# Performance work log

Measured on AMD Instinct MI355X. Metric: run time of the kernel, lower is better.

## Reference

```python
import jax, jax.numpy as jnp
import numpy as np

N = 50000   # num_nodes
E = 400000  # num_edges
IN, HID, OUT, H = 128, 64, 128, 4
GAT_HID = HID * H  # 256
EPS = 1e-5
NEG_SLOPE = 0.2


def setup_inputs() -> dict:
    key = jax.random.key(0)
    ks = jax.random.split(key, 24)

    def w(k, shape, fan_in):
        return (jax.random.normal(k, shape) * (1.0 / np.sqrt(fan_in))).astype(jnp.float32)

    x = jax.random.normal(ks[0], (N, IN), dtype=jnp.float32)
    edge_index = jax.random.randint(ks[1], (2, E), 0, N, dtype=jnp.int32)

    return {
        "x": x,
        "edge_index": edge_index,
        # GCN branch: layer1 IN->HID, layer2 HID->OUT
        "W_gcn1": w(ks[2], (IN, HID), IN), "b_gcn1": jnp.zeros((HID,), jnp.float32),
        "W_gcn2": w(ks[3], (HID, OUT), HID), "b_gcn2": jnp.zeros((OUT,), jnp.float32),
        # GAT branch: layer1 IN -> H heads x HID (concat), layer2 GAT_HID -> H heads x OUT (mean)
        "W_gat1": w(ks[4], (IN, H * HID), IN),
        "a_src1": w(ks[5], (H, HID), HID), "a_dst1": w(ks[6], (H, HID), HID),
        "b_gat1": jnp.zeros((H * HID,), jnp.float32),
        "W_gat2": w(ks[7], (GAT_HID, H * OUT), GAT_HID),
        "a_src2": w(ks[8], (H, OUT), OUT), "a_dst2": w(ks[9], (H, OUT), OUT),
        "b_gat2": jnp.zeros((OUT,), jnp.float32),
        # LayerNorms
        "g_gcn": jnp.ones((OUT,), jnp.float32), "bt_gcn": jnp.zeros((OUT,), jnp.float32),
        "g_gat": jnp.ones((OUT,), jnp.float32), "bt_gat": jnp.zeros((OUT,), jnp.float32),
        # projected_concat fusion
        "W_fuse": w(ks[10], (2 * OUT, OUT), 2 * OUT), "b_fuse": jnp.zeros((OUT,), jnp.float32),
    }


def _with_self_loops(src, dst, n):
    loop = jnp.arange(n, dtype=src.dtype)
    return jnp.concatenate([src, loop]), jnp.concatenate([dst, loop])


def _gcn_layer(x, W, b, src, dst, n):
    # PyG GCNConv: x' = D^{-1/2}(A+I)D^{-1/2} X W + b
    xw = x @ W
    s, d = _with_self_loops(src, dst, n)
    deg = jax.ops.segment_sum(jnp.ones_like(s, dtype=xw.dtype), d, num_segments=n)
    dis = jnp.where(deg > 0, jax.lax.rsqrt(jnp.maximum(deg, 1.0)), 0.0)
    norm = dis[s] * dis[d]                      # [E2]
    msg = norm[:, None] * xw[s]                 # [E2, C]
    return jax.ops.segment_sum(msg, d, num_segments=n) + b


def _segment_softmax(e, seg, n):
    m = jax.ops.segment_max(e, seg, num_segments=n)
    ee = jnp.exp(e - m[seg])
    den = jax.ops.segment_sum(ee, seg, num_segments=n)
    return ee / den[seg]


def _gat_layer(x, W, a_src, a_dst, b, src, dst, n, heads, out_ch, concat):
    xh = (x @ W).reshape(n, heads, out_ch)      # [N, H, C]
    alpha_s = jnp.einsum('nhc,hc->nh', xh, a_src)
    alpha_d = jnp.einsum('nhc,hc->nh', xh, a_dst)
    s, d = _with_self_loops(src, dst, n)
    e = jax.nn.leaky_relu(alpha_s[s] + alpha_d[d], NEG_SLOPE)   # [E2, H]
    alpha = _segment_softmax(e, d, n)                           # [E2, H]
    out = jax.ops.segment_sum(alpha[:, :, None] * xh[s], d, num_segments=n)  # [N,H,C]
    if concat:
        return out.reshape(n, heads * out_ch) + b
    return out.mean(axis=1) + b


def _layer_norm(x, g, b):
    mu = x.mean(axis=-1, keepdims=True)
    var = ((x - mu) ** 2).mean(axis=-1, keepdims=True)
    return (x - mu) * jax.lax.rsqrt(var + EPS) * g + b


def reference(x, edge_index,
              W_gcn1, b_gcn1, W_gcn2, b_gcn2,
              W_gat1, a_src1, a_dst1, b_gat1,
              W_gat2, a_src2, a_dst2, b_gat2,
              g_gcn, bt_gcn, g_gat, bt_gat,
              W_fuse, b_fuse):
    src, dst = edge_index[0], edge_index[1]
    n = x.shape[0]
    # GCN branch (relu between layers, dropout p=0.0 -> identity)
    h = jax.nn.relu(_gcn_layer(x, W_gcn1, b_gcn1, src, dst, n))
    x_gcn = _gcn_layer(h, W_gcn2, b_gcn2, src, dst, n)
    # GAT branch (elu between layers)
    g1 = _gat_layer(x, W_gat1, a_src1, a_dst1, b_gat1, src, dst, n, H, HID, True)
    g1 = jax.nn.elu(g1)
    x_gat = _gat_layer(g1, W_gat2, a_src2, a_dst2, b_gat2, src, dst, n, H, OUT, False)
    # Norm + projected_concat fusion
    x_gcn = _layer_norm(x_gcn, g_gcn, bt_gcn)
    x_gat = _layer_norm(x_gat, g_gat, bt_gat)
    x_cat = jnp.concatenate([x_gcn, x_gat], axis=-1)
    return x_cat @ W_fuse + b_fuse
```

## Files before the change

kernel.cpp:

```cpp
#include <hip/hip_runtime.h>
#include <cmath>

static constexpr float EPS = 1e-5f;
static constexpr float NEG = 0.2f;

typedef __attribute__((ext_vector_type(8))) short short8v;
typedef __attribute__((ext_vector_type(4))) short short4v;
typedef __attribute__((ext_vector_type(4))) float f32x4;

__device__ inline unsigned short f2bf(float f) {
    union { float f; unsigned u; } v; v.f = f;
    unsigned r = v.u + 0x7FFF + ((v.u >> 16) & 1);
    return (unsigned short)(r >> 16);
}
__device__ inline float bf2f(unsigned short u) {
    union { unsigned u; float f; } v; v.u = (unsigned)u << 16; return v.f;
}

__global__ void setup_kernel(const int* __restrict__ ei, int* __restrict__ cnt, int E, int n,
                             const float* __restrict__ x, unsigned short* __restrict__ xb,
                             const float* W1, const float* W2, const float* W3,
                             const float* W4, const float* W5,
                             unsigned short* T1, unsigned short* T2, unsigned short* T3,
                             unsigned short* TF, unsigned short* T5,
                             const float* as1, const float* ad1,
                             const float* as2, const float* ad2,
                             float* wa1, float* wa2) {
    int gid = blockIdx.x * 256 + threadIdx.x;
    if (gid < E) {
        atomicAdd(&cnt[ei[E + gid]], 1);
        return;
    }
    gid -= E;
    int n32 = n * 32;
    if (gid < n32) {
        float4 v = *reinterpret_cast<const float4*>(&x[(size_t)gid * 4]);
        unsigned long long pk = (unsigned long long)f2bf(v.x)
                              | ((unsigned long long)f2bf(v.y) << 16)
                              | ((unsigned long long)f2bf(v.z) << 32)
                              | ((unsigned long long)f2bf(v.w) << 48);
        *reinterpret_cast<unsigned long long*>(&xb[(size_t)gid * 4]) = pk;
        return;
    }
    gid -= n32;
    if (gid < 212992) {
        int idx = gid;
        if (idx < 8192) {
            int c = idx / 128, k = idx % 128;
            T1[idx] = f2bf(W1[(size_t)k * 64 + c]);
        } else if (idx < 16384) {
            int j = idx - 8192, c = j / 64, k = j % 64;
            T2[j] = f2bf(W2[(size_t)k * 128 + c]);
        } else if (idx < 49152) {
            int j = idx - 16384, c = j / 128, k = j % 128;
            T3[j] = f2bf(W3[(size_t)k * 256 + c]);
        } else if (idx < 180224) {
            int j = idx - 49152;
            int c = j / 1024, kk = j % 1024, h = kk >> 8, k = kk & 255;
            TF[j] = f2bf(0.25f * W4[(size_t)k * 512 + h * 128 + c]);
        } else {
            int j = idx - 180224, c = j / 256, k = j % 256;
            T5[j] = f2bf(W5[(size_t)k * 128 + c]);
        }
        return;
    }
    gid -= 212992;
    if (gid < 1024) {
        int k = gid >> 3, t = gid & 7, h = t >> 1;
        const float* a = (t & 1) ? ad1 : as1;
        float s = 0.f;
        for (int c = 0; c < 64; c++) s += W3[(size_t)k * 256 + h * 64 + c] * a[h * 64 + c];
        wa1[gid] = s;
    } else if (gid < 3072) {
        int j = gid - 1024;
        int k = j >> 3, t = j & 7, h = t >> 1;
        const float* a = (t & 1) ? ad2 : as2;
        float s = 0.f;
        for (int c = 0; c < 128; c++) s += W4[(size_t)k * 512 + h * 128 + c] * a[h * 128 + c];
        wa2[j] = s;
    }
}

__global__ __launch_bounds__(256) void partial_kernel(const int* __restrict__ cnt,
                                                      int* __restrict__ partials, int n) {
    int tid = threadIdx.x, lane = tid & 63, wid = tid >> 6;
    int base = blockIdx.x * 1024 + tid * 4;
    int s = 0;
    if (base + 3 < n) {
        int4 v = *reinterpret_cast<const int4*>(&cnt[base]);
        s = v.x + v.y + v.z + v.w;
    } else {
        for (int j = 0; j < 4; j++) if (base + j < n) s += cnt[base + j];
    }
    #pragma unroll
    for (int o = 32; o; o >>= 1) s += __shfl_xor(s, o, 64);
    __shared__ int ws[4];
    if (lane == 0) ws[wid] = s;
    __syncthreads();
    if (tid == 0) partials[blockIdx.x] = ws[0] + ws[1] + ws[2] + ws[3];
}

__global__ void scanp_kernel(int* __restrict__ partials, int nb) {
    int lane = threadIdx.x;
    int v = (lane < nb) ? partials[lane] : 0;
    int s = v;
    #pragma unroll
    for (int o = 1; o < 64; o <<= 1) {
        int t = __shfl_up(s, o, 64);
        if (lane >= o) s += t;
    }
    if (lane < nb) partials[lane] = s - v;
}

__global__ __launch_bounds__(256) void scan2_kernel(const int* __restrict__ cnt,
                                                    const int* __restrict__ partials,
                                                    int* __restrict__ rowptr,
                                                    int* __restrict__ cursor,
                                                    float* __restrict__ dis, int n, int E) {
    int tid = threadIdx.x, lane = tid & 63, wid = tid >> 6;
    int base = blockIdx.x * 1024 + tid * 4;
    int v[4]; int s = 0;
    #pragma unroll
    for (int j = 0; j < 4; j++) { v[j] = (base + j < n) ? cnt[base + j] : 0; s += v[j]; }
    int ts = s;
    #pragma unroll
    for (int o = 1; o < 64; o <<= 1) {
        int t = __shfl_up(ts, o, 64);
        if (lane >= o) ts += t;
    }
    __shared__ int wsum[4];
    if (lane == 63) wsum[wid] = ts;
    __syncthreads();
    int woff = 0;
    for (int w = 0; w < wid; w++) woff += wsum[w];
    int excl = ts - s + woff + partials[blockIdx.x];
    #pragma unroll
    for (int j = 0; j < 4; j++) {
        int idx = base + j;
        if (idx < n) {
            rowptr[idx] = excl;
            cursor[idx] = excl;
            dis[idx] = rsqrtf((float)(v[j] + 1));
            excl += v[j];
        }
    }
    if (blockIdx.x == 0 && tid == 0) rowptr[n] = E;
}

__global__ void fill_kernel(const int* __restrict__ ei, int* __restrict__ cursor,
                            int* __restrict__ col, int E) {
    int e = blockIdx.x * 256 + threadIdx.x;
    if (e < E) {
        int d = ei[E + e];
        int pos = atomicAdd(&cursor[d], 1);
        col[pos] = ei[e];
    }
}

template<int BM, int K, int C, bool OBF>
__global__ __launch_bounds__(256) void mfma_gemm(const unsigned short* __restrict__ A,
                                                 const unsigned short* __restrict__ WT,
                                                 const float* __restrict__ bias,
                                                 void* __restrict__ outp, int M) {
    constexpr int BN = 64, BK = 64;
    constexpr int MF = BM / 64;
    __shared__ unsigned short As[BM * BK];
    __shared__ unsigned short Ws[BN * BK];
    int tid = threadIdx.x;
    int wid = tid >> 6, lane = tid & 63;
    int m0 = blockIdx.x * BM;
    int n0 = blockIdx.y * BN;

    f32x4 acc[MF][4] = {};

    for (int k0 = 0; k0 < K; k0 += BK) {
        for (int i = tid; i < BM * (BK / 8); i += 256) {
            int row = i >> 3;
            int kk = (i & 7) * 8;
            int gr = m0 + row;
            short8v v = short8v{0, 0, 0, 0, 0, 0, 0, 0};
            if (gr < M) v = *reinterpret_cast<const short8v*>(&A[(size_t)gr * K + k0 + kk]);
            int byte = (kk * 2) ^ ((row & 7) << 4);
            *reinterpret_cast<short8v*>((char*)As + row * (BK * 2) + byte) = v;
        }
        for (int i = tid; i < BN * (BK / 8); i += 256) {
            int nrow = i >> 3;
            int kk = (i & 7) * 8;
            short8v v = *reinterpret_cast<const short8v*>(&WT[(size_t)(n0 + nrow) * K + k0 + kk]);
            int byte = (kk * 2) ^ ((nrow & 7) << 4);
            *reinterpret_cast<short8v*>((char*)Ws + nrow * (BK * 2) + byte) = v;
        }
        __syncthreads();
        #pragma unroll
        for (int kc = 0; kc < BK; kc += 32) {
            short8v afr[MF], bfr[4];
            int kk = kc + (lane >> 4) * 8;
            #pragma unroll
            for (int mf = 0; mf < MF; mf++) {
                int row = wid * (16 * MF) + mf * 16 + (lane & 15);
                int byte = (kk * 2) ^ ((row & 7) << 4);
                afr[mf] = *reinterpret_cast<const short8v*>((char*)As + row * (BK * 2) + byte);
            }
            #pragma unroll
            for (int nf = 0; nf < 4; nf++) {
                int nrow = nf * 16 + (lane & 15);
                int byte = (kk * 2) ^ ((nrow & 7) << 4);
                bfr[nf] = *reinterpret_cast<const short8v*>((char*)Ws + nrow * (BK * 2) + byte);
            }
            #pragma unroll
            for (int mf = 0; mf < MF; mf++)
                #pragma unroll
                for (int nf = 0; nf < 4; nf++)
                    acc[mf][nf] = __builtin_amdgcn_mfma_f32_16x16x32_bf16(
                        afr[mf], bfr[nf], acc[mf][nf], 0, 0, 0);
        }
        __syncthreads();
    }
    #pragma unroll
    for (int mf = 0; mf < MF; mf++) {
        #pragma unroll
        for (int nf = 0; nf < 4; nf++) {
            #pragma unroll
            for (int r = 0; r < 4; r++) {
                int row = m0 + wid * (16 * MF) + mf * 16 + (lane >> 4) * 4 + r;
                int colg = n0 + nf * 16 + (lane & 15);
                if (row < M) {
                    float v = acc[mf][nf][r];
                    if (bias) v += bias[colg];
                    if constexpr (OBF)
                        ((unsigned short*)outp)[(size_t)row * C + colg] = f2bf(v);
                    else
                        ((float*)outp)[(size_t)row * C + colg] = v;
                }
            }
        }
    }
}

__global__ __launch_bounds__(256) void gemm_head_kernel(const unsigned short* __restrict__ A,
                                                        const unsigned short* __restrict__ WT3,
                                                        const float* __restrict__ bias,
                                                        unsigned short* __restrict__ g1b, int M) {
    constexpr int BM = 64, BK = 64, K = 128;
    int head = blockIdx.y;
    __shared__ unsigned short As[BM * BK];
    __shared__ unsigned short Ws[64 * BK];
    int tid = threadIdx.x;
    int wid = tid >> 6, lane = tid & 63;
    int m0 = blockIdx.x * BM;

    f32x4 acc[4] = {};

    for (int k0 = 0; k0 < K; k0 += BK) {
        for (int i = tid; i < BM * (BK / 8); i += 256) {
            int row = i >> 3;
            int kk = (i & 7) * 8;
            int gr = m0 + row;
            short8v v = short8v{0, 0, 0, 0, 0, 0, 0, 0};
            if (gr < M) v = *reinterpret_cast<const short8v*>(&A[(size_t)gr * 512 + head * 128 + k0 + kk]);
            int byte = (kk * 2) ^ ((row & 7) << 4);
            *reinterpret_cast<short8v*>((char*)As + row * (BK * 2) + byte) = v;
        }
        for (int i = tid; i < 64 * (BK / 8); i += 256) {
            int nrow = i >> 3;
            int kk = (i & 7) * 8;
            short8v v = *reinterpret_cast<const short8v*>(&WT3[(size_t)(head * 64 + nrow) * 128 + k0 + kk]);
            int byte = (kk * 2) ^ ((nrow & 7) << 4);
            *reinterpret_cast<short8v*>((char*)Ws + nrow * (BK * 2) + byte) = v;
        }
        __syncthreads();
        #pragma unroll
        for (int kc = 0; kc < BK; kc += 32) {
            short8v afr, bfr[4];
            int kk = kc + (lane >> 4) * 8;
            {
                int row = wid * 16 + (lane & 15);
                int byte = (kk * 2) ^ ((row & 7) << 4);
                afr = *reinterpret_cast<const short8v*>((char*)As + row * (BK * 2) + byte);
            }
            #pragma unroll
            for (int nf = 0; nf < 4; nf++) {
                int nrow = nf * 16 + (lane & 15);
                int byte = (kk * 2) ^ ((nrow & 7) << 4);
                bfr[nf] = *reinterpret_cast<const short8v*>((char*)Ws + nrow * (BK * 2) + byte);
            }
            #pragma unroll
            for (int nf = 0; nf < 4; nf++)
                acc[nf] = __builtin_amdgcn_mfma_f32_16x16x32_bf16(afr, bfr[nf], acc[nf], 0, 0, 0);
        }
        __syncthreads();
    }
    #pragma unroll
    for (int nf = 0; nf < 4; nf++) {
        #pragma unroll
        for (int r = 0; r < 4; r++) {
            int row = m0 + wid * 16 + (lane >> 4) * 4 + r;
            int cl = head * 64 + nf * 16 + (lane & 15);
            if (row < M) {
                float v = acc[nf][r] + bias[cl];
                v = v > 0.f ? v : __expf(v) - 1.f;
                g1b[(size_t)row * 256 + cl] = f2bf(v);
            }
        }
    }
}

template<int K>
__global__ __launch_bounds__(256) void gemm_ln_kernel(const unsigned short* __restrict__ A,
                                                      const unsigned short* __restrict__ WT,
                                                      const float* __restrict__ bias,
                                                      const float* __restrict__ gw,
                                                      const float* __restrict__ gb,
                                                      unsigned short* __restrict__ catb,
                                                      int coloff, int M) {
    constexpr int BM = 64, BN = 128, BK = 64;
    __shared__ unsigned short As[BM * BK];
    __shared__ unsigned short Ws[BN * BK];
    int tid = threadIdx.x;
    int wid = tid >> 6, lane = tid & 63;
    int m0 = blockIdx.x * BM;

    f32x4 acc[8] = {};

    for (int k0 = 0; k0 < K; k0 += BK) {
        for (int i = tid; i < BM * (BK / 8); i += 256) {
            int row = i >> 3;
            int kk = (i & 7) * 8;
            int gr = m0 + row;
            short8v v = short8v{0, 0, 0, 0, 0, 0, 0, 0};
            if (gr < M) v = *reinterpret_cast<const short8v*>(&A[(size_t)gr * K + k0 + kk]);
            int byte = (kk * 2) ^ ((row & 7) << 4);
            *reinterpret_cast<short8v*>((char*)As + row * (BK * 2) + byte) = v;
        }
        for (int i = tid; i < BN * (BK / 8); i += 256) {
            int nrow = i >> 3;
            int kk = (i & 7) * 8;
            short8v v = *reinterpret_cast<const short8v*>(&WT[(size_t)nrow * K + k0 + kk]);
            int byte = (kk * 2) ^ ((nrow & 7) << 4);
            *reinterpret_cast<short8v*>((char*)Ws + nrow * (BK * 2) + byte) = v;
        }
        __syncthreads();
        #pragma unroll
        for (int kc = 0; kc < BK; kc += 32) {
            short8v afr, bfr[8];
            int kk = kc + (lane >> 4) * 8;
            {
                int row = wid * 16 + (lane & 15);
                int byte = (kk * 2) ^ ((row & 7) << 4);
                afr = *reinterpret_cast<const short8v*>((char*)As + row * (BK * 2) + byte);
            }
            #pragma unroll
            for (int nf = 0; nf < 8; nf++) {
                int nrow = nf * 16 + (lane & 15);
                int byte = (kk * 2) ^ ((nrow & 7) << 4);
                bfr[nf] = *reinterpret_cast<const short8v*>((char*)Ws + nrow * (BK * 2) + byte);
            }
            #pragma unroll
            for (int nf = 0; nf < 8; nf++)
                acc[nf] = __builtin_amdgcn_mfma_f32_16x16x32_bf16(afr, bfr[nf], acc[nf], 0, 0, 0);
        }
        __syncthreads();
    }
    int cb = lane & 15;
    float gwv[8], gbv[8], bv[8];
    #pragma unroll
    for (int nf = 0; nf < 8; nf++) {
        int c = nf * 16 + cb;
        gwv[nf] = gw[c]; gbv[nf] = gb[c]; bv[nf] = bias[c];
    }
    #pragma unroll
    for (int r = 0; r < 4; r++) {
        int row = m0 + wid * 16 + (lane >> 4) * 4 + r;
        float v[8]; float sm = 0.f, sq = 0.f;
        #pragma unroll
        for (int nf = 0; nf < 8; nf++) {
            v[nf] = acc[nf][r] + bv[nf];
            sm += v[nf]; sq += v[nf] * v[nf];
        }
        #pragma unroll
        for (int o = 1; o < 16; o <<= 1) { sm += __shfl_xor(sm, o, 64); sq += __shfl_xor(sq, o, 64); }
        float mu = sm * (1.f / 128.f);
        float var = sq * (1.f / 128.f) - mu * mu;
        float rs = rsqrtf(var + EPS);
        if (row < M) {
            #pragma unroll
            for (int nf = 0; nf < 8; nf++)
                catb[(size_t)row * 256 + coloff + nf * 16 + cb] =
                    f2bf((v[nf] - mu) * rs * gwv[nf] + gbv[nf]);
        }
    }
}

template<int K>
__global__ __launch_bounds__(256) void alpha_x_kernel(const unsigned short* __restrict__ F,
                                                      const float* __restrict__ wa,
                                                      float* __restrict__ as_, float* __restrict__ ad_, int n) {
    constexpr int PL = K / 64;
    int wid = threadIdx.x >> 6, lane = threadIdx.x & 63;
    int node = blockIdx.x * 4 + wid;
    if (node >= n) return;
    float p[8] = {0, 0, 0, 0, 0, 0, 0, 0};
    const unsigned short* fr = F + (size_t)node * K + lane * PL;
    #pragma unroll
    for (int j = 0; j < PL; j++) {
        float v = bf2f(fr[j]);
        const float4* w4 = reinterpret_cast<const float4*>(wa + (size_t)(lane * PL + j) * 8);
        float4 wA = w4[0], wB = w4[1];
        p[0] += v * wA.x; p[1] += v * wA.y; p[2] += v * wA.z; p[3] += v * wA.w;
        p[4] += v * wB.x; p[5] += v * wB.y; p[6] += v * wB.z; p[7] += v * wB.w;
    }
    #pragma unroll
    for (int o = 1; o < 64; o <<= 1) {
        #pragma unroll
        for (int t = 0; t < 8; t++) p[t] += __shfl_xor(p[t], o, 64);
    }
    if (lane == 0) {
        #pragma unroll
        for (int t = 0; t < 8; t++) {
            if (t & 1) ad_[(size_t)node * 4 + (t >> 1)] = p[t];
            else       as_[(size_t)node * 4 + (t >> 1)] = p[t];
        }
    }
}

__global__ __launch_bounds__(256) void prop1_agg1_kernel(const unsigned short* __restrict__ xb,
                                                         const unsigned short* __restrict__ xw,
                                                         const float* __restrict__ dis,
                                                         const float* __restrict__ as_,
                                                         const float* __restrict__ ad_,
                                                         const int* __restrict__ rowptr,
                                                         const int* __restrict__ col,
                                                         const float* __restrict__ bias,
                                                         unsigned short* __restrict__ hb,
                                                         unsigned short* __restrict__ agg,
                                                         int n) {
    constexpr int CAP = 96;
    __shared__ float ex[4][CAP][4];
    __shared__ int scol[4][CAP];
    int wid = threadIdx.x >> 6, lane = threadIdx.x & 63;
    int node = blockIdx.x * 4 + wid;
    if (node >= n) return;
    int b0 = rowptr[node];
    int cnt = rowptr[node + 1] - b0;
    float4 adv = *reinterpret_cast<const float4*>(&ad_[(size_t)node * 4]);
    float p0 = 0, p1 = 0, p2 = 0, p3 = 0;
    for (int i = lane; i <= cnt; i += 64) {
        int s = (i == cnt) ? node : col[b0 + i];
        float4 asv = *reinterpret_cast<const float4*>(&as_[(size_t)s * 4]);
        float e0 = asv.x + adv.x; e0 = e0 > 0.f ? e0 : NEG * e0; float x0 = __expf(e0);
        float e1 = asv.y + adv.y; e1 = e1 > 0.f ? e1 : NEG * e1; float x1 = __expf(e1);
        float e2 = asv.z + adv.z; e2 = e2 > 0.f ? e2 : NEG * e2; float x2 = __expf(e2);
        float e3 = asv.w + adv.w; e3 = e3 > 0.f ? e3 : NEG * e3; float x3 = __expf(e3);
        if (i < CAP) {
            ex[wid][i][0] = x0; ex[wid][i][1] = x1; ex[wid][i][2] = x2; ex[wid][i][3] = x3;
            scol[wid][i] = s;
        }
        p0 += x0; p1 += x1; p2 += x2; p3 += x3;
    }
    #pragma unroll
    for (int o = 1; o < 64; o <<= 1) {
        p0 += __shfl_xor(p0, o, 64); p1 += __shfl_xor(p1, o, 64);
        p2 += __shfl_xor(p2, o, 64); p3 += __shfl_xor(p3, o, 64);
    }
    __builtin_amdgcn_wave_barrier();
    float inv0 = 1.f / p0, inv1 = 1.f / p1, inv2 = 1.f / p2, inv3 = 1.f / p3;
    float gacc = 0.f;
    float ac[4][2] = {};
    for (int i = 0; i <= cnt; i++) {
        int s; float w0, w1, w2, w3;
        if (i < CAP) {
            s = scol[wid][i];
            float4 e = *reinterpret_cast<const float4*>(&ex[wid][i][0]);
            w0 = e.x * inv0; w1 = e.y * inv1; w2 = e.z * inv2; w3 = e.w * inv3;
        } else {
            s = (i == cnt) ? node : col[b0 + i];
            float4 asv = *reinterpret_cast<const float4*>(&as_[(size_t)s * 4]);
            float e0 = asv.x + adv.x; e0 = e0 > 0.f ? e0 : NEG * e0;
            float e1 = asv.y + adv.y; e1 = e1 > 0.f ? e1 : NEG * e1;
            float e2 = asv.z + adv.z; e2 = e2 > 0.f ? e2 : NEG * e2;
            float e3 = asv.w + adv.w; e3 = e3 > 0.f ? e3 : NEG * e3;
            w0 = __expf(e0) * inv0; w1 = __expf(e1) * inv1;
            w2 = __expf(e2) * inv2; w3 = __expf(e3) * inv3;
        }
        float ds = dis[s];
        unsigned gv = *reinterpret_cast<const unsigned*>(&xb[(size_t)s * 128 + lane * 2]);
        float xv = bf2f(xw[(size_t)s * 64 + lane]);
        gacc += ds * xv;
        float f0 = bf2f((unsigned short)(gv & 0xFFFF));
        float f1 = bf2f((unsigned short)(gv >> 16));
        ac[0][0] += w0 * f0; ac[0][1] += w0 * f1;
        ac[1][0] += w1 * f0; ac[1][1] += w1 * f1;
        ac[2][0] += w2 * f0; ac[2][1] += w2 * f1;
        ac[3][0] += w3 * f0; ac[3][1] += w3 * f1;
    }
    float dd = dis[node];
    float r = dd * gacc + bias[lane];
    r = fmaxf(r, 0.f);
    hb[(size_t)node * 64 + lane] = f2bf(r);
    #pragma unroll
    for (int h = 0; h < 4; h++) {
        unsigned pk = (unsigned)f2bf(ac[h][0]) | ((unsigned)f2bf(ac[h][1]) << 16);
        *reinterpret_cast<unsigned*>(&agg[(size_t)node * 512 + h * 128 + lane * 2]) = pk;
    }
}

__global__ __launch_bounds__(256) void prop2_agg2_kernel(const unsigned short* __restrict__ g1b,
                                                         const unsigned short* __restrict__ xw2,
                                                         const float* __restrict__ dis,
                                                         const float* __restrict__ as_,
                                                         const float* __restrict__ ad_,
                                                         const int* __restrict__ rowptr,
                                                         const int* __restrict__ col,
                                                         const float* __restrict__ bias,
                                                         const float* __restrict__ gw,
                                                         const float* __restrict__ gb,
                                                         unsigned short* __restrict__ catb,
                                                         unsigned short* __restrict__ agg,
                                                         int n) {
    constexpr int CAP = 96;
    __shared__ float ex[4][CAP][4];
    __shared__ int scol[4][CAP];
    int wid = threadIdx.x >> 6, lane = threadIdx.x & 63;
    int node = blockIdx.x * 4 + wid;
    if (node >= n) return;
    int b0 = rowptr[node];
    int cnt = rowptr[node + 1] - b0;
    float4 adv = *reinterpret_cast<const float4*>(&ad_[(size_t)node * 4]);
    float p0 = 0, p1 = 0, p2 = 0, p3 = 0;
    for (int i = lane; i <= cnt; i += 64) {
        int s = (i == cnt) ? node : col[b0 + i];
        float4 asv = *reinterpret_cast<const float4*>(&as_[(size_t)s * 4]);
        float e0 = asv.x + adv.x; e0 = e0 > 0.f ? e0 : NEG * e0; float x0 = __expf(e0);
        float e1 = asv.y + adv.y; e1 = e1 > 0.f ? e1 : NEG * e1; float x1 = __expf(e1);
        float e2 = asv.z + adv.z; e2 = e2 > 0.f ? e2 : NEG * e2; float x2 = __expf(e2);
        float e3 = asv.w + adv.w; e3 = e3 > 0.f ? e3 : NEG * e3; float x3 = __expf(e3);
        if (i < CAP) {
            ex[wid][i][0] = x0; ex[wid][i][1] = x1; ex[wid][i][2] = x2; ex[wid][i][3] = x3;
            scol[wid][i] = s;
        }
        p0 += x0; p1 += x1; p2 += x2; p3 += x3;
    }
    #pragma unroll
    for (int o = 1; o < 64; o <<= 1) {
        p0 += __shfl_xor(p0, o, 64); p1 += __shfl_xor(p1, o, 64);
        p2 += __shfl_xor(p2, o, 64); p3 += __shfl_xor(p3, o, 64);
    }
    __builtin_amdgcn_wave_barrier();
    float inv0 = 1.f / p0, inv1 = 1.f / p1, inv2 = 1.f / p2, inv3 = 1.f / p3;
    float a0 = 0.f, a1 = 0.f;
    float ac[4][4] = {};
    for (int i = 0; i <= cnt; i++) {
        int s; float w0, w1, w2, w3;
        if (i < CAP) {
            s = scol[wid][i];
            float4 e = *reinterpret_cast<const float4*>(&ex[wid][i][0]);
            w0 = e.x * inv0; w1 = e.y * inv1; w2 = e.z * inv2; w3 = e.w * inv3;
        } else {
            s = (i == cnt) ? node : col[b0 + i];
            float4 asv = *reinterpret_cast<const float4*>(&as_[(size_t)s * 4]);
            float e0 = asv.x + adv.x; e0 = e0 > 0.f ? e0 : NEG * e0;
            float e1 = asv.y + adv.y; e1 = e1 > 0.f ? e1 : NEG * e1;
            float e2 = asv.z + adv.z; e2 = e2 > 0.f ? e2 : NEG * e2;
            float e3 = asv.w + adv.w; e3 = e3 > 0.f ? e3 : NEG * e3;
            w0 = __expf(e0) * inv0; w1 = __expf(e1) * inv1;
            w2 = __expf(e2) * inv2; w3 = __expf(e3) * inv3;
        }
        float ds = dis[s];
        short4v v = *reinterpret_cast<const short4v*>(&g1b[(size_t)s * 256 + lane * 4]);
        unsigned gv = *reinterpret_cast<const unsigned*>(&xw2[(size_t)s * 128 + lane * 2]);
        a0 += ds * bf2f((unsigned short)(gv & 0xFFFF));
        a1 += ds * bf2f((unsigned short)(gv >> 16));
        float f0 = bf2f((unsigned short)v[0]);
        float f1 = bf2f((unsigned short)v[1]);
        float f2 = bf2f((unsigned short)v[2]);
        float f3 = bf2f((unsigned short)v[3]);
        ac[0][0] += w0 * f0; ac[0][1] += w0 * f1; ac[0][2] += w0 * f2; ac[0][3] += w0 * f3;
        ac[1][0] += w1 * f0; ac[1][1] += w1 * f1; ac[1][2] += w1 * f2; ac[1][3] += w1 * f3;
        ac[2][0] += w2 * f0; ac[2][1] += w2 * f1; ac[2][2] += w2 * f2; ac[2][3] += w2 * f3;
        ac[3][0] += w3 * f0; ac[3][1] += w3 * f1; ac[3][2] += w3 * f2; ac[3][3] += w3 * f3;
    }
    float dd = dis[node];
    float r0 = dd * a0 + bias[lane * 2];
    float r1 = dd * a1 + bias[lane * 2 + 1];
    float sm = r0 + r1, sq = r0 * r0 + r1 * r1;
    #pragma unroll
    for (int o = 1; o < 64; o <<= 1) { sm += __shfl_xor(sm, o, 64); sq += __shfl_xor(sq, o, 64); }
    float mu = sm * (1.f / 128.f);
    float var = sq * (1.f / 128.f) - mu * mu;
    float rs = rsqrtf(var + EPS);
    float o0 = (r0 - mu) * rs * gw[lane * 2] + gb[lane * 2];
    float o1 = (r1 - mu) * rs * gw[lane * 2 + 1] + gb[lane * 2 + 1];
    unsigned pk = (unsigned)f2bf(o0) | ((unsigned)f2bf(o1) << 16);
    *reinterpret_cast<unsigned*>(&catb[(size_t)node * 256 + lane * 2]) = pk;
    #pragma unroll
    for (int h = 0; h < 4; h++) {
        short4v o4;
        o4[0] = (short)f2bf(ac[h][0]); o4[1] = (short)f2bf(ac[h][1]);
        o4[2] = (short)f2bf(ac[h][2]); o4[3] = (short)f2bf(ac[h][3]);
        *reinterpret_cast<short4v*>(&agg[(size_t)node * 1024 + h * 256 + lane * 4]) = o4;
    }
}

extern "C" void kernel_launch(void* const* d_in, const int* in_sizes, int n_in,
                              void* d_out, int out_size, void* d_ws, size_t ws_size,
                              hipStream_t stream) {
    const float* x      = (const float*)d_in[0];
    const int*   ei     = (const int*)d_in[1];
    const float* W_gcn1 = (const float*)d_in[2];
    const float* b_gcn1 = (const float*)d_in[3];
    const float* W_gcn2 = (const float*)d_in[4];
    const float* b_gcn2 = (const float*)d_in[5];
    const float* W_gat1 = (const float*)d_in[6];
    const float* a_src1 = (const float*)d_in[7];
    const float* a_dst1 = (const float*)d_in[8];
    const float* b_gat1 = (const float*)d_in[9];
    const float* W_gat2 = (const float*)d_in[10];
    const float* a_src2 = (const float*)d_in[11];
    const float* a_dst2 = (const float*)d_in[12];
    const float* b_gat2 = (const float*)d_in[13];
    const float* g_gcn  = (const float*)d_in[14];
    const float* bt_gcn = (const float*)d_in[15];
    const float* g_gat  = (const float*)d_in[16];
    const float* bt_gat = (const float*)d_in[17];
    const float* W_fuse = (const float*)d_in[18];
    const float* b_fuse = (const float*)d_in[19];
    float* out = (float*)d_out;

    const int n = in_sizes[0] / 128;
    const int E = in_sizes[1] / 2;

    char* ws = (char*)d_ws;
    size_t off = 0;
    auto alloc = [&](size_t bytes) -> char* {
        char* p = ws + off;
        off += (bytes + 255) & ~(size_t)255;
        return p;
    };
    int*   cnt      = (int*)alloc((size_t)n * 4);
    int*   rowptr   = (int*)alloc((size_t)(n + 1) * 4);
    int*   cursor   = (int*)alloc((size_t)n * 4);
    int*   col      = (int*)alloc((size_t)E * 4);
    int*   partials = (int*)alloc(64 * 4);
    float* dis      = (float*)alloc((size_t)n * 4);
    float* as_      = (float*)alloc((size_t)n * 16);
    float* ad_      = (float*)alloc((size_t)n * 16);
    float* wa1      = (float*)alloc(1024 * 4);
    float* wa2      = (float*)alloc(2048 * 4);
    unsigned short* xb   = (unsigned short*)alloc((size_t)n * 128 * 2);
    unsigned short* WT1  = (unsigned short*)alloc(8192 * 2);
    unsigned short* WT2  = (unsigned short*)alloc(8192 * 2);
    unsigned short* WT3  = (unsigned short*)alloc(32768 * 2);
    unsigned short* WTF  = (unsigned short*)alloc(131072 * 2);
    unsigned short* WT5  = (unsigned short*)alloc(32768 * 2);
    unsigned short* BIG   = (unsigned short*)alloc((size_t)n * 1024 * 2);
    unsigned short* agg2b = BIG;
    unsigned short* agg1b = BIG;
    unsigned short* xw1b  = BIG + (size_t)n * 512;
    unsigned short* hb    = BIG + (size_t)n * 576;
    unsigned short* xw2b  = (unsigned short*)alloc((size_t)n * 128 * 2);
    unsigned short* g1b   = (unsigned short*)alloc((size_t)n * 256 * 2);
    unsigned short* catb  = (unsigned short*)alloc((size_t)n * 256 * 2);

    const int nb = (n + 1023) / 1024;

    hipMemsetAsync(cnt, 0, (size_t)n * 4, stream);
    {
        long long total = (long long)E + (long long)n * 32 + 212992 + 3072;
        int blocks = (int)((total + 255) / 256);
        setup_kernel<<<blocks, 256, 0, stream>>>(ei, cnt, E, n, x, xb,
            W_gcn1, W_gcn2, W_gat1, W_gat2, W_fuse, WT1, WT2, WT3, WTF, WT5,
            a_src1, a_dst1, a_src2, a_dst2, wa1, wa2);
    }
    partial_kernel<<<nb, 256, 0, stream>>>(cnt, partials, n);
    scanp_kernel<<<1, 64, 0, stream>>>(partials, nb);
    scan2_kernel<<<nb, 256, 0, stream>>>(cnt, partials, rowptr, cursor, dis, n, E);
    fill_kernel<<<(E + 255) / 256, 256, 0, stream>>>(ei, cursor, col, E);

    int gm64 = (n + 63) / 64;
    int gn4 = (n + 3) / 4;

    mfma_gemm<64, 128, 64, true><<<dim3(gm64, 1), 256, 0, stream>>>(xb, WT1, nullptr, xw1b, n);
    alpha_x_kernel<128><<<gn4, 256, 0, stream>>>(xb, wa1, as_, ad_, n);
    prop1_agg1_kernel<<<gn4, 256, 0, stream>>>(xb, xw1b, dis, as_, ad_, rowptr, col,
                                               b_gcn1, hb, agg1b, n);
    mfma_gemm<64, 64, 128, true><<<dim3(gm64, 2), 256, 0, stream>>>(hb, WT2, nullptr, xw2b, n);
    gemm_head_kernel<<<dim3(gm64, 4), 256, 0, stream>>>(agg1b, WT3, b_gat1, g1b, n);
    alpha_x_kernel<256><<<gn4, 256, 0, stream>>>(g1b, wa2, as_, ad_, n);
    prop2_agg2_kernel<<<gn4, 256, 0, stream>>>(g1b, xw2b, dis, as_, ad_, rowptr, col,
                                               b_gcn2, g_gcn, bt_gcn, catb, agg2b, n);
    gemm_ln_kernel<1024><<<gm64, 256, 0, stream>>>(agg2b, WTF, b_gat2, g_gat, bt_gat, catb, 128, n);

    mfma_gemm<64, 256, 128, false><<<dim3(gm64, 2), 256, 0, stream>>>(catb, WT5, b_fuse, out, n);
}
```

Before: 354.8 us.

## Reorder GCN layers to aggregate before projecting, moving LayerNorm into a GEMM

Each GCN layer now aggregates over neighbours before multiplying by the weight matrix, using (A X) W instead of A (X W). Layer 1 aggregates the raw 128-wide input in the GAT-1 propagation kernel, then a GEMM with fused bias and ReLU produces h. Layer 2 aggregates the 64-wide h and then runs gemm_ln<64> to do the projection plus LayerNorm. This narrows the per-edge gather in layer 2 from 128 to 64 channels and drops a standalone GEMM from before propagation. In exchange, layer 1 now gathers 128 channels instead of 64, and the launch adds an extra GEMM+LN kernel.

Result: faster. 346.2 us (-2.4%).

```diff
diff --git a/kernel.cpp b/kernel.cpp
--- a/kernel.cpp
+++ b/kernel.cpp
@@ -157,7 +157,7 @@
     }
 }
 
-template<int BM, int K, int C, bool OBF>
+template<int BM, int K, int C, bool OBF, int ACT>
 __global__ __launch_bounds__(256) void mfma_gemm(const unsigned short* __restrict__ A,
                                                  const unsigned short* __restrict__ WT,
                                                  const float* __restrict__ bias,
@@ -227,6 +227,7 @@
                 if (row < M) {
                     float v = acc[mf][nf][r];
                     if (bias) v += bias[colg];
+                    if (ACT == 1) v = fmaxf(v, 0.f);
                     if constexpr (OBF)
                         ((unsigned short*)outp)[(size_t)row * C + colg] = f2bf(v);
                     else
@@ -424,14 +425,12 @@
 }
 
 __global__ __launch_bounds__(256) void prop1_agg1_kernel(const unsigned short* __restrict__ xb,
-                                                         const unsigned short* __restrict__ xw,
                                                          const float* __restrict__ dis,
                                                          const float* __restrict__ as_,
                                                          const float* __restrict__ ad_,
                                                          const int* __restrict__ rowptr,
                                                          const int* __restrict__ col,
-                                                         const float* __restrict__ bias,
-                                                         unsigned short* __restrict__ hb,
+                                                         unsigned short* __restrict__ aggx,
                                                          unsigned short* __restrict__ agg,
                                                          int n) {
     constexpr int CAP = 96;
@@ -464,7 +463,7 @@
     }
     __builtin_amdgcn_wave_barrier();
     float inv0 = 1.f / p0, inv1 = 1.f / p1, inv2 = 1.f / p2, inv3 = 1.f / p3;
-    float gacc = 0.f;
+    float g0 = 0.f, g1 = 0.f;
     float ac[4][2] = {};
     for (int i = 0; i <= cnt; i++) {
         int s; float w0, w1, w2, w3;
@@ -484,19 +483,17 @@
         }
         float ds = dis[s];
         unsigned gv = *reinterpret_cast<const unsigned*>(&xb[(size_t)s * 128 + lane * 2]);
-        float xv = bf2f(xw[(size_t)s * 64 + lane]);
-        gacc += ds * xv;
         float f0 = bf2f((unsigned short)(gv & 0xFFFF));
         float f1 = bf2f((unsigned short)(gv >> 16));
+        g0 += ds * f0; g1 += ds * f1;
         ac[0][0] += w0 * f0; ac[0][1] += w0 * f1;
         ac[1][0] += w1 * f0; ac[1][1] += w1 * f1;
         ac[2][0] += w2 * f0; ac[2][1] += w2 * f1;
         ac[3][0] += w3 * f0; ac[3][1] += w3 * f1;
     }
     float dd = dis[node];
-    float r = dd * gacc + bias[lane];
-    r = fmaxf(r, 0.f);
-    hb[(size_t)node * 64 + lane] = f2bf(r);
+    unsigned pkg = (unsigned)f2bf(dd * g0) | ((unsigned)f2bf(dd * g1) << 16);
+    *reinterpret_cast<unsigned*>(&aggx[(size_t)node * 128 + lane * 2]) = pkg;
     #pragma unroll
     for (int h = 0; h < 4; h++) {
         unsigned pk = (unsigned)f2bf(ac[h][0]) | ((unsigned)f2bf(ac[h][1]) << 16);
@@ -505,16 +502,13 @@
 }
 
 __global__ __launch_bounds__(256) void prop2_agg2_kernel(const unsigned short* __restrict__ g1b,
-                                                         const unsigned short* __restrict__ xw2,
+                                                         const unsigned short* __restrict__ hb,
                                                          const float* __restrict__ dis,
                                                          const float* __restrict__ as_,
                                                          const float* __restrict__ ad_,
                                                          const int* __restrict__ rowptr,
                                                          const int* __restrict__ col,
-                                                         const float* __restrict__ bias,
-                                                         const float* __restrict__ gw,
-                                                         const float* __restrict__ gb,
-                                                         unsigned short* __restrict__ catb,
+                                                         unsigned short* __restrict__ aggh,
                                                          unsigned short* __restrict__ agg,
                                                          int n) {
     constexpr int CAP = 96;
@@ -547,7 +541,7 @@
     }
     __builtin_amdgcn_wave_barrier();
     float inv0 = 1.f / p0, inv1 = 1.f / p1, inv2 = 1.f / p2, inv3 = 1.f / p3;
-    float a0 = 0.f, a1 = 0.f;
+    float hacc = 0.f;
     float ac[4][4] = {};
     for (int i = 0; i <= cnt; i++) {
         int s; float w0, w1, w2, w3;
@@ -567,9 +561,8 @@
         }
         float ds = dis[s];
         short4v v = *reinterpret_cast<const short4v*>(&g1b[(size_t)s * 256 + lane * 4]);
-        unsigned gv = *reinterpret_cast<const unsigned*>(&xw2[(size_t)s * 128 + lane * 2]);
-        a0 += ds * bf2f((unsigned short)(gv & 0xFFFF));
-        a1 += ds * bf2f((unsigned short)(gv >> 16));
+        float hv = bf2f(hb[(size_t)s * 64 + lane]);
+        hacc += ds * hv;
         float f0 = bf2f((unsigned short)v[0]);
         float f1 = bf2f((unsigned short)v[1]);
         float f2 = bf2f((unsigned short)v[2]);
@@ -580,18 +573,7 @@
         ac[3][0] += w3 * f0; ac[3][1] += w3 * f1; ac[3][2] += w3 * f2; ac[3][3] += w3 * f3;
     }
     float dd = dis[node];
-    float r0 = dd * a0 + bias[lane * 2];
-    float r1 = dd * a1 + bias[lane * 2 + 1];
-    float sm = r0 + r1, sq = r0 * r0 + r1 * r1;
-    #pragma unroll
-    for (int o = 1; o < 64; o <<= 1) { sm += __shfl_xor(sm, o, 64); sq += __shfl_xor(sq, o, 64); }
-    float mu = sm * (1.f / 128.f);
-    float var = sq * (1.f / 128.f) - mu * mu;
-    float rs = rsqrtf(var + EPS);
-    float o0 = (r0 - mu) * rs * gw[lane * 2] + gb[lane * 2];
-    float o1 = (r1 - mu) * rs * gw[lane * 2 + 1] + gb[lane * 2 + 1];
-    unsigned pk = (unsigned)f2bf(o0) | ((unsigned)f2bf(o1) << 16);
-    *reinterpret_cast<unsigned*>(&catb[(size_t)node * 256 + lane * 2]) = pk;
+    aggh[(size_t)node * 64 + lane] = f2bf(dd * hacc);
     #pragma unroll
     for (int h = 0; h < 4; h++) {
         short4v o4;
@@ -655,9 +637,9 @@
     unsigned short* BIG   = (unsigned short*)alloc((size_t)n * 1024 * 2);
     unsigned short* agg2b = BIG;
     unsigned short* agg1b = BIG;
-    unsigned short* xw1b  = BIG + (size_t)n * 512;
-    unsigned short* hb    = BIG + (size_t)n * 576;
-    unsigned short* xw2b  = (unsigned short*)alloc((size_t)n * 128 * 2);
+    unsigned short* aggx1 = BIG + (size_t)n * 512;
+    unsigned short* hb    = (unsigned short*)alloc((size_t)n * 64 * 2);
+    unsigned short* aggh  = (unsigned short*)alloc((size_t)n * 64 * 2);
     unsigned short* g1b   = (unsigned short*)alloc((size_t)n * 256 * 2);
     unsigned short* catb  = (unsigned short*)alloc((size_t)n * 256 * 2);
 
@@ -679,16 +661,14 @@
     int gm64 = (n + 63) / 64;
     int gn4 = (n + 3) / 4;
 
-    mfma_gemm<64, 128, 64, true><<<dim3(gm64, 1), 256, 0, stream>>>(xb, WT1, nullptr, xw1b, n);
     alpha_x_kernel<128><<<gn4, 256, 0, stream>>>(xb, wa1, as_, ad_, n);
-    prop1_agg1_kernel<<<gn4, 256, 0, stream>>>(xb, xw1b, dis, as_, ad_, rowptr, col,
-                                               b_gcn1, hb, agg1b, n);
-    mfma_gemm<64, 64, 128, true><<<dim3(gm64, 2), 256, 0, stream>>>(hb, WT2, nullptr, xw2b, n);
+    prop1_agg1_kernel<<<gn4, 256, 0, stream>>>(xb, dis, as_, ad_, rowptr, col, aggx1, agg1b, n);
+    mfma_gemm<64, 128, 64, true, 1><<<dim3(gm64, 1), 256, 0, stream>>>(aggx1, WT1, b_gcn1, hb, n);
     gemm_head_kernel<<<dim3(gm64, 4), 256, 0, stream>>>(agg1b, WT3, b_gat1, g1b, n);
     alpha_x_kernel<256><<<gn4, 256, 0, stream>>>(g1b, wa2, as_, ad_, n);
-    prop2_agg2_kernel<<<gn4, 256, 0, stream>>>(g1b, xw2b, dis, as_, ad_, rowptr, col,
-                                               b_gcn2, g_gcn, bt_gcn, catb, agg2b, n);
+    prop2_agg2_kernel<<<gn4, 256, 0, stream>>>(g1b, hb, dis, as_, ad_, rowptr, col, aggh, agg2b, n);
+    gemm_ln_kernel<64><<<gm64, 256, 0, stream>>>(aggh, WT2, b_gcn2, g_gcn, bt_gcn, catb, 0, n);
     gemm_ln_kernel<1024><<<gm64, 256, 0, stream>>>(agg2b, WTF, b_gat2, g_gat, bt_gat, catb, 128, n);
 
-    mfma_gemm<64, 256, 128, false><<<dim3(gm64, 2), 256, 0, stream>>>(catb, WT5, b_fuse, out, n);
-}
+    mfma_gemm<64, 256, 128, false, 0><<<dim3(gm64, 2), 256, 0, stream>>>(catb, WT5, b_fuse, out, n);
+}
```
